# Kernel optimization log

Hardware: AMD Instinct MI355X
Metric: run time of the kernel (lower is better)

The kernel has to match this reference:

```python
import jax, jax.numpy as jnp
import numpy as np

HEADS = 16
HEAD_DIM = 64
EMB = 1024
B, S = 4, 2048
SCALE = 1.0 / 8.0  # fixed constant in the original code
MASK_PENALTY = -50.0  # original adds -50 * upper_triangular, not -inf


def setup_inputs() -> dict:
    key = jax.random.key(0)
    ks = jax.random.split(key, 5)
    x = jax.random.normal(ks[0], (B, S, EMB), dtype=jnp.float32)
    Wq = jax.random.normal(ks[1], (EMB, HEADS * HEAD_DIM), dtype=jnp.float32) * 0.02
    Wk = jax.random.normal(ks[2], (EMB, HEADS * HEAD_DIM), dtype=jnp.float32) * 0.02
    Wv = jax.random.normal(ks[3], (EMB, HEADS * HEAD_DIM), dtype=jnp.float32) * 0.02
    Wr = jax.random.normal(ks[4], (HEADS * HEAD_DIM, EMB), dtype=jnp.float32) * 0.02
    return {"x": x, "Wq": Wq, "Wk": Wk, "Wv": Wv, "Wr": Wr}


def reference(x, Wq, Wk, Wv, Wr):
    b, s, _ = x.shape
    # project and split heads: [b, s, h, d]
    q = (x @ Wq).reshape(b, s, HEADS, HEAD_DIM)
    k = (x @ Wk).reshape(b, s, HEADS, HEAD_DIM)
    v = (x @ Wv).reshape(b, s, HEADS, HEAD_DIM)
    # scores: [b, h, s, s]
    scores = SCALE * jnp.einsum('bqhd,bkhd->bhqk', q, k)
    # causal additive mask: -50 on strictly-upper triangle (faithful to original)
    causal = jnp.triu(jnp.ones((s, s), dtype=x.dtype), k=1)
    scores = scores + MASK_PENALTY * causal
    attn = jax.nn.softmax(scores, axis=-1)
    out = jnp.einsum('bhqk,bkhd->bqhd', attn, v).reshape(b, s, HEADS * HEAD_DIM)
    return out @ Wr
```

## Files before the change

kernel.cpp:

```cpp
#include <hip/hip_runtime.h>

typedef _Float16 f16;
typedef _Float16 f16x8 __attribute__((ext_vector_type(8)));
typedef _Float16 f16x4 __attribute__((ext_vector_type(4)));
typedef float f32x4 __attribute__((ext_vector_type(4)));

#define MFMA16(A, B, C) __builtin_amdgcn_mfma_f32_16x16x32_f16((A), (B), (C), 0, 0, 0)

__device__ __forceinline__ void async16(void* lds, const void* gp) {
    __builtin_amdgcn_global_load_lds(
        (__attribute__((address_space(1))) void*)(gp),
        (__attribute__((address_space(3))) void*)(lds), 16, 0, 0);
}

__global__ __launch_bounds__(256) void k_prep(const float* __restrict__ x,
                                              const float* __restrict__ Wq,
                                              const float* __restrict__ Wk,
                                              const float* __restrict__ Wv,
                                              const float* __restrict__ Wr,
                                              f16* __restrict__ xb,
                                              f16* __restrict__ Wqkvt,
                                              f16* __restrict__ Wrt) {
    __shared__ float tile[32][33];
    int bid = blockIdx.x;
    if (bid < 8192) {
        int i = (bid * 256 + threadIdx.x) * 4;
        float4 v = *(const float4*)(x + i);
        f16x4 o = {(f16)v.x, (f16)v.y, (f16)v.z, (f16)v.w};
        *(f16x4*)(xb + i) = o;
    } else {
        int wid = bid - 8192;
        int z = wid >> 10;
        int tid = wid & 1023;
        const float* W = (z == 0) ? Wq : (z == 1) ? Wk : (z == 2) ? Wv : Wr;
        f16* Wt = (z == 3) ? Wrt : Wqkvt + z * 1048576;
        int c0 = (tid & 31) * 32, r0 = (tid >> 5) * 32;
        int tx = threadIdx.x & 31, ty = threadIdx.x >> 5;
#pragma unroll
        for (int j = 0; j < 32; j += 8)
            tile[ty + j][tx] = W[(r0 + ty + j) * 1024 + c0 + tx];
        __syncthreads();
#pragma unroll
        for (int j = 0; j < 32; j += 8)
            Wt[(c0 + ty + j) * 1024 + r0 + tx] = (f16)tile[tx][ty + j];
    }
}

__global__ __launch_bounds__(256) void k_transpose_v(const f16* __restrict__ QKV,
                                                     f16* __restrict__ Vt) {
    __shared__ f16 tile[32][33];
    int s0 = blockIdx.x * 32;
    int d0 = blockIdx.y * 32;
    int bh = blockIdx.z;
    int b = bh >> 4, h = bh & 15;
    int tx = threadIdx.x, ty = threadIdx.y;
#pragma unroll
    for (int j = 0; j < 32; j += 8)
        tile[ty + j][tx] = QKV[(b * 2048 + s0 + ty + j) * 3072 + 2048 + h * 64 + d0 + tx];
    __syncthreads();
#pragma unroll
    for (int j = 0; j < 32; j += 8)
        Vt[(bh * 64 + d0 + ty + j) * 2048 + s0 + tx] = tile[tx][ty + j];
}

template <bool OUT_F16>
__global__ __launch_bounds__(256) void k_gemm_bt(const f16* __restrict__ A,
                                                 const f16* __restrict__ Bt,
                                                 void* __restrict__ Cv,
                                                 int M, int N, int K) {
    __shared__ f16 As[3][128][32];
    __shared__ f16 Bs[3][128][32];
    int t = threadIdx.x;
    int lane = t & 63, w = t >> 6;
    int wm = (w >> 1) * 64, wn = (w & 1) * 64;
    int m0 = blockIdx.y * 128, n0 = blockIdx.x * 128;
    int ln = lane & 15, g = lane >> 4;

    int lin0 = w * 128 + lane, lin1 = lin0 + 64;
    int r0 = lin0 >> 2, c0 = (lin0 & 3) ^ ((r0 >> 1) & 3);
    int r1 = lin1 >> 2, c1 = (lin1 & 3) ^ ((r1 >> 1) & 3);
    const f16* gA0 = A + (size_t)(m0 + r0) * K + c0 * 8;
    const f16* gA1 = A + (size_t)(m0 + r1) * K + c1 * 8;
    const f16* gB0 = Bt + (size_t)(n0 + r0) * K + c0 * 8;
    const f16* gB1 = Bt + (size_t)(n0 + r1) * K + c1 * 8;

    f32x4 acc[4][4] = {};
    int sw = (ln >> 1) & 3;

#define GISSUE(bi, kk)                                    \
    do {                                                  \
        f16* lA = &As[0][0][0] + (bi) * 4096 + w * 1024;  \
        f16* lB = &Bs[0][0][0] + (bi) * 4096 + w * 1024;  \
        async16(lA, gA0 + (kk));                          \
        async16(lA + 512, gA1 + (kk));                    \
        async16(lB, gB0 + (kk));                          \
        async16(lB + 512, gB1 + (kk));                    \
    } while (0)

    GISSUE(0, 0);
    GISSUE(1, 32);

    int b0 = 0, b1 = 1, b2 = 2;
    for (int k0 = 0; k0 < K; k0 += 32) {
        if (k0 + 32 < K)
            asm volatile("s_waitcnt vmcnt(4) lgkmcnt(0)" ::: "memory");
        else
            asm volatile("s_waitcnt vmcnt(0) lgkmcnt(0)" ::: "memory");
        __builtin_amdgcn_s_barrier();
        __builtin_amdgcn_sched_barrier(0);
        if (k0 + 64 < K) GISSUE(b2, k0 + 64);

        f16x8 af[4], bf[4];
#pragma unroll
        for (int i = 0; i < 4; i++) {
            af[i] = *(const f16x8*)&As[b0][wm + i * 16 + ln][(g ^ sw) * 8];
            bf[i] = *(const f16x8*)&Bs[b0][wn + i * 16 + ln][(g ^ sw) * 8];
        }
#pragma unroll
        for (int mt = 0; mt < 4; mt++)
#pragma unroll
            for (int nt = 0; nt < 4; nt++)
                acc[mt][nt] = MFMA16(af[mt], bf[nt], acc[mt][nt]);

        int tmp = b0; b0 = b1; b1 = b2; b2 = tmp;
    }
#undef GISSUE

    int rg = g * 4;
#pragma unroll
    for (int mt = 0; mt < 4; mt++)
#pragma unroll
        for (int nt = 0; nt < 4; nt++)
#pragma unroll
            for (int r = 0; r < 4; r++) {
                int row = m0 + wm + mt * 16 + rg + r;
                int col = n0 + wn + nt * 16 + ln;
                float v = acc[mt][nt][r];
                if (OUT_F16)
                    ((f16*)Cv)[(size_t)row * N + col] = (f16)v;
                else
                    ((float*)Cv)[(size_t)row * N + col] = v;
            }
}

__global__ __launch_bounds__(256, 2) void k_attn(const f16* __restrict__ QKV,
                                                 const f16* __restrict__ Vt,
                                                 f16* __restrict__ Opart,
                                                 float* __restrict__ Rsum) {
    __shared__ f16 Ks[2][64][64];
    __shared__ f16 Vs[2][64][64];
    int bh = blockIdx.x, pi = blockIdx.y;
    int b = bh >> 4, h = bh & 15;
    int t = threadIdx.x, lane = t & 63, wq = t >> 6;
    int ln = lane & 15, g = lane >> 4, g8 = g * 8, rg = g * 4;
    int sx = ln & 7;

    int r0 = wq * 8 + (lane >> 3);
    int cp = lane & 7;
    int cl = (cp ^ (r0 & 7)) * 8;
    int gk0 = ((r0 & 16) >> 2) | ((r0 & 12) << 1) | (r0 & 3);
    const f16* Kb = QKV + (size_t)b * 2048 * 3072 + 1024 + h * 64;
    const f16* Vb = Vt + (size_t)bh * 64 * 2048;
    const f16* gK0 = Kb + (size_t)gk0 * 3072 + cl;
    const f16* gK1 = Kb + (size_t)(gk0 + 32) * 3072 + cl;
    const f16* gV0 = Vb + (size_t)r0 * 2048 + cl;
    const f16* gV1 = Vb + (size_t)(r0 + 32) * 2048 + cl;

    const float C_SCL = 0.18033688f;
    const float C_MSK = -72.134752f;
    f16x8 ones;
#pragma unroll
    for (int j = 0; j < 8; j++) ones[j] = (f16)1.f;

    int nk0 = 16 - pi;

#define ISSUE(bi, j)                                                      \
    do {                                                                  \
        int jj = (j);                                                     \
        int kt_ = (jj < nk0) ? jj : jj - nk0 + pi + 1;                    \
        size_t kO = (size_t)kt_ * 64;                                     \
        async16(&Ks[bi][wq * 8][0],      gK0 + kO * 3072);                \
        async16(&Ks[bi][32 + wq * 8][0], gK1 + kO * 3072);                \
        async16(&Vs[bi][wq * 8][0],      gV0 + kO);                       \
        async16(&Vs[bi][32 + wq * 8][0], gV1 + kO);                       \
    } while (0)

    ISSUE(0, 0);
    __syncthreads();

    int i = 0;
    for (int phase = 0; phase < 2; phase++) {
        int qt  = phase ? pi : 15 - pi;
        int ktB = phase ? pi + 1 : 0;
        int ktE = phase ? 2 * pi + 2 : 16 - pi;
        int q0 = qt * 128;

        f16x8 bq[2][2];
#pragma unroll
        for (int nt = 0; nt < 2; nt++)
#pragma unroll
            for (int kd = 0; kd < 2; kd++)
                bq[nt][kd] = *(const f16x8*)(QKV +
                    (size_t)(b * 2048 + q0 + wq * 32 + nt * 16 + ln) * 3072 +
                    h * 64 + kd * 32 + g8);

        f32x4 oacc[2][4] = {};
        f32x4 osum[2] = {};

        for (int kt = ktB; kt < ktE; kt++, i++) {
            int cur = i & 1;
            int k0 = kt * 64;
            bool active = (k0 <= q0 + wq * 32 + 31);

            if (i + 1 < 17) ISSUE(cur ^ 1, i + 1);

            if (active) {
                f16x8 ak[2][4];
#pragma unroll
                for (int kd = 0; kd < 2; kd++)
#pragma unroll
                    for (int mt = 0; mt < 4; mt++)
                        ak[kd][mt] = *(const f16x8*)
                            &Ks[cur][mt * 16 + ln][((kd * 4 + g) ^ sx) * 8];
                f32x4 sacc[4][2] = {};
#pragma unroll
                for (int kd = 0; kd < 2; kd++)
#pragma unroll
                    for (int mt = 0; mt < 4; mt++)
#pragma unroll
                        for (int nt = 0; nt < 2; nt++)
                            sacc[mt][nt] = MFMA16(ak[kd][mt], bq[nt][kd], sacc[mt][nt]);

                bool needs_mask = (k0 + 63 > q0 + wq * 32);
                f16x8 ap[2][2];
#pragma unroll
                for (int nt = 0; nt < 2; nt++) {
                    int q = q0 + wq * 32 + nt * 16 + ln;
#pragma unroll
                    for (int mt = 0; mt < 4; mt++) {
                        int kb = mt >> 1, hi4 = (mt & 1) * 4;
#pragma unroll
                        for (int r = 0; r < 4; r++) {
                            float e;
                            if (needs_mask) {
                                int kk = k0 + kb * 32 + hi4 + 8 * g + r;
                                e = __builtin_amdgcn_exp2f(
                                    fmaf(sacc[mt][nt][r], C_SCL, (kk > q) ? C_MSK : 0.f));
                            } else {
                                e = __builtin_amdgcn_exp2f(sacc[mt][nt][r] * C_SCL);
                            }
                            ap[nt][kb][hi4 + r] = (f16)e;
                        }
                    }
                }

#pragma unroll
                for (int kk = 0; kk < 2; kk++) {
                    f16x8 bv[4];
#pragma unroll
                    for (int dt = 0; dt < 4; dt++)
                        bv[dt] = *(const f16x8*)
                            &Vs[cur][dt * 16 + ln][((kk * 4 + g) ^ sx) * 8];
#pragma unroll
                    for (int nt = 0; nt < 2; nt++) {
#pragma unroll
                        for (int dt = 0; dt < 4; dt++)
                            oacc[nt][dt] = MFMA16(ap[nt][kk], bv[dt], oacc[nt][dt]);
                        osum[nt] = MFMA16(ap[nt][kk], ones, osum[nt]);
                    }
                }
            }
            __syncthreads();
        }

        int u = (bh * 16 + qt) * 2 + phase;
#pragma unroll
        for (int nt = 0; nt < 2; nt++)
#pragma unroll
            for (int r = 0; r < 4; r++) {
                float rs = osum[nt][r];
                float inv = __builtin_amdgcn_rcpf(fmaxf(rs, 1e-30f));
                int q = wq * 32 + nt * 16 + rg + r;
                if (ln == 0) Rsum[u * 128 + q] = rs;
#pragma unroll
                for (int dt = 0; dt < 4; dt++)
                    Opart[(size_t)u * 8192 + q * 64 + dt * 16 + ln] =
                        (f16)(oacc[nt][dt][r] * inv);
            }
    }
#undef ISSUE
}

__global__ __launch_bounds__(256) void k_merge(const f16* __restrict__ Op,
                                               const float* __restrict__ Rs,
                                               f16* __restrict__ Ob) {
    int idx = blockIdx.x * 256 + threadIdx.x;
    int d8 = idx & 7;
    int q  = (idx >> 3) & 127;
    int qt = (idx >> 10) & 15;
    int bh = idx >> 14;
    int b = bh >> 4, hd = bh & 15;
    int u0 = (bh * 16 + qt) * 2;
    float rs0 = Rs[u0 * 128 + q], rs1 = Rs[(u0 + 1) * 128 + q];
    float inv = __builtin_amdgcn_rcpf(rs0 + rs1);
    f16x8 o0 = *(const f16x8*)(Op + (size_t)u0 * 8192 + q * 64 + d8 * 8);
    f16x8 o1 = *(const f16x8*)(Op + (size_t)(u0 + 1) * 8192 + q * 64 + d8 * 8);
    f16x8 o;
#pragma unroll
    for (int j = 0; j < 8; j++)
        o[j] = (f16)((rs0 * (float)o0[j] + rs1 * (float)o1[j]) * inv);
    *(f16x8*)(Ob + (size_t)(b * 2048 + qt * 128 + q) * 1024 + hd * 64 + d8 * 8) = o;
}

extern "C" void kernel_launch(void* const* d_in, const int* in_sizes, int n_in,
                              void* d_out, int out_size, void* d_ws, size_t ws_size,
                              hipStream_t stream) {
    const float* x = (const float*)d_in[0];
    const float* Wq = (const float*)d_in[1];
    const float* Wk = (const float*)d_in[2];
    const float* Wv = (const float*)d_in[3];
    const float* Wr = (const float*)d_in[4];
    float* out = (float*)d_out;

    f16* ws = (f16*)d_ws;
    f16* xb    = ws;
    f16* Wqkvt = xb + 8388608;
    f16* Wrt   = Wqkvt + 3145728;
    f16* QKVb  = Wrt + 1048576;
    f16* Vtb   = QKVb + 25165824;
    f16* Obuf  = Vtb + 8388608;
    f16* Opart = Obuf + 8388608;
    float* Rsum = (float*)(Opart + 16777216);

    k_prep<<<12288, 256, 0, stream>>>(x, Wq, Wk, Wv, Wr, xb, Wqkvt, Wrt);
    k_gemm_bt<true><<<dim3(24, 64), 256, 0, stream>>>(xb, Wqkvt, QKVb, 8192, 3072, 1024);
    dim3 tb(32, 8);
    k_transpose_v<<<dim3(64, 2, 64), tb, 0, stream>>>(QKVb, Vtb);
    k_attn<<<dim3(64, 16), 256, 0, stream>>>(QKVb, Vtb, Opart, Rsum);
    k_merge<<<4096, 256, 0, stream>>>(Opart, Rsum, Obuf);
    k_gemm_bt<false><<<dim3(8, 64), 256, 0, stream>>>(Obuf, Wrt, out, 8192, 1024, 1024);
}
```

Measured before the change: 270.2 us.

## Fuse split-KV partial merge into output projection GEMM A-tile loads

Removes the separate merge kernel and the Obuf round trip. The output projection GEMM now reads the two attention partial outputs and their row sums directly, combines them in registers, and writes the merged fp16 A tile into LDS, while B still arrives by async global-to-LDS loads. This saves one launch and a write plus read of an 8M-element fp16 buffer. In exchange, each of the 8 N-column blocks redoes the merge, so Opart (twice the size of Obuf) is read 8 times, and A loads become register-staged instead of async.

```diff
diff --git a/kernel.cpp b/kernel.cpp
--- a/kernel.cpp
+++ b/kernel.cpp
@@ -143,6 +143,117 @@
             }
 }
 
+__global__ __launch_bounds__(256) void k_gemm_merge(const f16* __restrict__ Opart,
+                                                    const float* __restrict__ Rsum,
+                                                    const f16* __restrict__ Bt,
+                                                    float* __restrict__ C) {
+    const int K = 1024, N = 1024;
+    __shared__ f16 As[2][128][32];
+    __shared__ f16 Bs[2][128][32];
+    int t = threadIdx.x;
+    int lane = t & 63, w = t >> 6;
+    int wm = (w >> 1) * 64, wn = (w & 1) * 64;
+    int m0 = blockIdx.y * 128, n0 = blockIdx.x * 128;
+    int ln = lane & 15, g = lane >> 4;
+
+    int lin0 = w * 128 + lane, lin1 = lin0 + 64;
+    int r0 = lin0 >> 2, c0 = (lin0 & 3) ^ ((r0 >> 1) & 3);
+    int r1 = lin1 >> 2, c1 = (lin1 & 3) ^ ((r1 >> 1) & 3);
+    const f16* gB0 = Bt + (size_t)(n0 + r0) * K + c0 * 8;
+    const f16* gB1 = Bt + (size_t)(n0 + r1) * K + c1 * 8;
+
+    int ubase = (m0 >> 11) * 512 + ((m0 >> 7) & 15) * 2;
+
+    f32x4 acc[4][4] = {};
+    int sw = (ln >> 1) & 3;
+
+    int4 ra00, ra01, ra10, ra11;
+    float rs00, rs01, rs10, rs11;
+
+#define ALOAD(kk)                                                             \
+    do {                                                                      \
+        int h_ = (kk) >> 6;                                                   \
+        size_t u0_ = ubase + h_ * 32;                                         \
+        int d0_ = ((kk) & 63) + c0 * 8, d1_ = ((kk) & 63) + c1 * 8;           \
+        ra00 = *(const int4*)(Opart + u0_ * 8192 + r0 * 64 + d0_);            \
+        ra01 = *(const int4*)(Opart + (u0_ + 1) * 8192 + r0 * 64 + d0_);      \
+        ra10 = *(const int4*)(Opart + u0_ * 8192 + r1 * 64 + d1_);            \
+        ra11 = *(const int4*)(Opart + (u0_ + 1) * 8192 + r1 * 64 + d1_);      \
+        rs00 = Rsum[u0_ * 128 + r0];                                          \
+        rs01 = Rsum[(u0_ + 1) * 128 + r0];                                    \
+        rs10 = Rsum[u0_ * 128 + r1];                                          \
+        rs11 = Rsum[(u0_ + 1) * 128 + r1];                                    \
+    } while (0)
+
+#define AWRITE(bi)                                                            \
+    do {                                                                      \
+        float i0_ = __builtin_amdgcn_rcpf(rs00 + rs01);                       \
+        float i1_ = __builtin_amdgcn_rcpf(rs10 + rs11);                       \
+        float s00 = rs00 * i0_, s01 = rs01 * i0_;                             \
+        float s10 = rs10 * i1_, s11 = rs11 * i1_;                             \
+        f16x8 o0 = *(f16x8*)&ra00, o1 = *(f16x8*)&ra01;                       \
+        f16x8 p0 = *(f16x8*)&ra10, p1 = *(f16x8*)&ra11;                       \
+        f16x8 m0v, m1v;                                                       \
+        _Pragma("unroll") for (int e = 0; e < 8; e++) {                       \
+            m0v[e] = (f16)(s00 * (float)o0[e] + s01 * (float)o1[e]);          \
+            m1v[e] = (f16)(s10 * (float)p0[e] + s11 * (float)p1[e]);          \
+        }                                                                     \
+        *(f16x8*)(&As[bi][0][0] + lin0 * 8) = m0v;                            \
+        *(f16x8*)(&As[bi][0][0] + lin1 * 8) = m1v;                            \
+    } while (0)
+
+#define BISSUE(bi, kk)                                    \
+    do {                                                  \
+        f16* lB = &Bs[bi][0][0] + w * 1024;               \
+        async16(lB, gB0 + (kk));                          \
+        async16(lB + 512, gB1 + (kk));                    \
+    } while (0)
+
+    ALOAD(0);
+    BISSUE(0, 0);
+    AWRITE(0);
+    ALOAD(32);
+    __syncthreads();
+
+    int cur = 0;
+    for (int k0 = 0; k0 < K; k0 += 32) {
+        if (k0 + 32 < K) {
+            AWRITE(cur ^ 1);
+            BISSUE(cur ^ 1, k0 + 32);
+        }
+        if (k0 + 64 < K) ALOAD(k0 + 64);
+
+        f16x8 af[4], bf[4];
+#pragma unroll
+        for (int i = 0; i < 4; i++) {
+            af[i] = *(const f16x8*)&As[cur][wm + i * 16 + ln][(g ^ sw) * 8];
+            bf[i] = *(const f16x8*)&Bs[cur][wn + i * 16 + ln][(g ^ sw) * 8];
+        }
+#pragma unroll
+        for (int mt = 0; mt < 4; mt++)
+#pragma unroll
+            for (int nt = 0; nt < 4; nt++)
+                acc[mt][nt] = MFMA16(af[mt], bf[nt], acc[mt][nt]);
+        __syncthreads();
+        cur ^= 1;
+    }
+#undef ALOAD
+#undef AWRITE
+#undef BISSUE
+
+    int rg = g * 4;
+#pragma unroll
+    for (int mt = 0; mt < 4; mt++)
+#pragma unroll
+        for (int nt = 0; nt < 4; nt++)
+#pragma unroll
+            for (int r = 0; r < 4; r++) {
+                int row = m0 + wm + mt * 16 + rg + r;
+                int col = n0 + wn + nt * 16 + ln;
+                C[(size_t)row * N + col] = acc[mt][nt][r];
+            }
+}
+
 __global__ __launch_bounds__(256, 2) void k_attn(const f16* __restrict__ QKV,
                                                  const f16* __restrict__ Vt,
                                                  f16* __restrict__ Opart,
@@ -291,27 +402,6 @@
 #undef ISSUE
 }
 
-__global__ __launch_bounds__(256) void k_merge(const f16* __restrict__ Op,
-                                               const float* __restrict__ Rs,
-                                               f16* __restrict__ Ob) {
-    int idx = blockIdx.x * 256 + threadIdx.x;
-    int d8 = idx & 7;
-    int q  = (idx >> 3) & 127;
-    int qt = (idx >> 10) & 15;
-    int bh = idx >> 14;
-    int b = bh >> 4, hd = bh & 15;
-    int u0 = (bh * 16 + qt) * 2;
-    float rs0 = Rs[u0 * 128 + q], rs1 = Rs[(u0 + 1) * 128 + q];
-    float inv = __builtin_amdgcn_rcpf(rs0 + rs1);
-    f16x8 o0 = *(const f16x8*)(Op + (size_t)u0 * 8192 + q * 64 + d8 * 8);
-    f16x8 o1 = *(const f16x8*)(Op + (size_t)(u0 + 1) * 8192 + q * 64 + d8 * 8);
-    f16x8 o;
-#pragma unroll
-    for (int j = 0; j < 8; j++)
-        o[j] = (f16)((rs0 * (float)o0[j] + rs1 * (float)o1[j]) * inv);
-    *(f16x8*)(Ob + (size_t)(b * 2048 + qt * 128 + q) * 1024 + hd * 64 + d8 * 8) = o;
-}
-
 extern "C" void kernel_launch(void* const* d_in, const int* in_sizes, int n_in,
                               void* d_out, int out_size, void* d_ws, size_t ws_size,
                               hipStream_t stream) {
@@ -337,6 +427,5 @@
     dim3 tb(32, 8);
     k_transpose_v<<<dim3(64, 2, 64), tb, 0, stream>>>(QKVb, Vtb);
     k_attn<<<dim3(64, 16), 256, 0, stream>>>(QKVb, Vtb, Opart, Rsum);
-    k_merge<<<4096, 256, 0, stream>>>(Opart, Rsum, Obuf);
-    k_gemm_bt<false><<<dim3(8, 64), 256, 0, stream>>>(Obuf, Wrt, out, 8192, 1024, 1024);
-}
+    k_gemm_merge<<<dim3(8, 64), 256, 0, stream>>>(Opart, Rsum, Wrt, out);
+}
```

Result: slower. 288.5 us (+6.8%).
